# Performance work log

Hardware: AMD Instinct MI355X
Metric: run time of the kernel (lower is better)

The kernel has to match this reference:

```python
import jax, jax.numpy as jnp
import numpy as np

N = 100000   # nodes
E = 1600000  # edges
F = 128      # input features
H = 128      # hidden channels
G = 64       # graphs in batch
EPS = 1e-5   # BatchNorm eps


def setup_inputs() -> dict:
    key = jax.random.key(0)
    ks = jax.random.split(key, 24)
    s = 0.05
    d = {}
    d["x"] = jax.random.normal(ks[0], (N, F), jnp.float32)
    d["edge_index"] = jax.random.randint(ks[1], (2, E), 0, N, dtype=jnp.int32)
    d["batch"] = jnp.sort(jax.random.randint(ks[2], (N,), 0, G, dtype=jnp.int32))
    # GCNConv weights/biases
    d["W1"] = jax.random.normal(ks[3], (F, H), jnp.float32) * s
    d["b1"] = jnp.zeros((H,), jnp.float32)
    d["W2"] = jax.random.normal(ks[4], (H, H), jnp.float32) * s
    d["b2"] = jnp.zeros((H,), jnp.float32)
    d["W3"] = jax.random.normal(ks[5], (H, H), jnp.float32) * s
    d["b3"] = jnp.zeros((H,), jnp.float32)
    # BatchNorm affine params
    for i, k in zip((1, 2, 3), (ks[6], ks[7], ks[8])):
        d[f"g{i}"] = jnp.ones((H,), jnp.float32) + jax.random.normal(k, (H,), jnp.float32) * 0.01
        d[f"be{i}"] = jnp.zeros((H,), jnp.float32)
    # MLP: Linear(2H, H) -> ReLU -> Linear(H, 1)
    d["Wm1"] = jax.random.normal(ks[9], (2 * H, H), jnp.float32) * s
    d["bm1"] = jnp.zeros((H,), jnp.float32)
    d["Wm2"] = jax.random.normal(ks[10], (H, 1), jnp.float32) * s
    d["bm2"] = jnp.zeros((1,), jnp.float32)
    return d


def _gcn_conv(x, W, b, src, dst, dinv):
    # PyG GCNConv: h = D^{-1/2}(A+I)D^{-1/2} (x W) + b, with self-loops
    h = x @ W                                   # [N, H]
    norm = (dinv[src] * dinv[dst])[:, None]     # [E, 1]
    agg = jax.ops.segment_sum(h[src] * norm, dst, num_segments=N)
    agg = agg + h * (dinv * dinv)[:, None]      # self-loop term
    return agg + b


def _bn(x, g, be):
    # BatchNorm1d, training-mode batch stats (biased variance), over node dim
    m = jnp.mean(x, axis=0)
    v = jnp.var(x, axis=0)
    return (x - m) * jax.lax.rsqrt(v + EPS) * g + be


def reference(x, W1, b1, g1, be1, W2, b2, g2, be2, W3, b3, g3, be3,
              Wm1, bm1, Wm2, bm2, edge_index, batch):
    src, dst = edge_index[0], edge_index[1]
    # degree with self-loops (edge weight 1)
    deg = jax.ops.segment_sum(jnp.ones((E,), x.dtype), dst, num_segments=N) + 1.0
    dinv = jax.lax.rsqrt(deg)

    h = jax.nn.relu(_bn(_gcn_conv(x, W1, b1, src, dst, dinv), g1, be1))  # dropout(p=0.05) = identity in eval
    res = h
    h = jax.nn.relu(_bn(_gcn_conv(h, W2, b2, src, dst, dinv), g2, be2)) + res
    res = h
    h = jax.nn.relu(_bn(_gcn_conv(h, W3, b3, src, dst, dinv), g3, be3)) + res

    x_sum = jax.ops.segment_sum(h, batch, num_segments=G)                 # [G, H]
    cnt = jax.ops.segment_sum(jnp.ones((N,), h.dtype), batch, num_segments=G)
    x_mean = x_sum / jnp.maximum(cnt, 1.0)[:, None]
    z = jnp.concatenate([x_sum, x_mean], axis=-1)                         # [G, 2H]
    z = jax.nn.relu(z @ Wm1 + bm1)
    return z @ Wm2 + bm2                                                  # [G, 1]
```

## Files before the change

### kernel.cpp

```cpp
#include <hip/hip_runtime.h>

#define NN 100000
#define EE 1600000
#define HD 128
#define GG 64
#define NB 391
#define BNEPS 1e-5f

typedef unsigned int uint_t;
typedef unsigned short ushort_t;
typedef __attribute__((ext_vector_type(8))) short bf16x8;
typedef __attribute__((ext_vector_type(4))) float f32x4;

static __device__ __forceinline__ ushort_t f2bf(float f){
  uint_t b = __float_as_uint(f);
  return (ushort_t)((b + 0x7FFFu + ((b >> 16) & 1u)) >> 16);
}
static __device__ __forceinline__ uint_t pack2bf(float a, float b){
  return (uint_t)f2bf(a) | ((uint_t)f2bf(b) << 16);
}
static __device__ __forceinline__ float bflo(uint_t u){ return __uint_as_float(u << 16); }
static __device__ __forceinline__ float bfhi(uint_t u){ return __uint_as_float(u & 0xFFFF0000u); }

__global__ void k_hist(const int* __restrict__ ei, int* __restrict__ cnt){
  int e = blockIdx.x*256 + threadIdx.x;
  if (e < EE) atomicAdd(&cnt[ei[EE + e]], 1);
}

__global__ void k_scanA(const int* __restrict__ cnt, int* __restrict__ offs,
                        int* __restrict__ bsum, float* __restrict__ dinv){
  __shared__ int s[256];
  int tid = threadIdx.x;
  int n = blockIdx.x*256 + tid;
  int v = (n < NN) ? cnt[n] : 0;
  if (n < NN) dinv[n] = rsqrtf(1.0f + (float)v);
  s[tid] = v; __syncthreads();
  for (int d = 1; d < 256; d <<= 1){
    int t = (tid >= d) ? s[tid-d] : 0;
    __syncthreads();
    s[tid] += t;
    __syncthreads();
  }
  if (n < NN) offs[n] = s[tid] - v;
  if (tid == 255) bsum[blockIdx.x] = s[255];
}

__global__ void k_scanB(int* __restrict__ bsum){
  __shared__ int s[512];
  int tid = threadIdx.x;
  int v = (tid < NB) ? bsum[tid] : 0;
  s[tid] = v; __syncthreads();
  for (int d = 1; d < 512; d <<= 1){
    int t = (tid >= d) ? s[tid-d] : 0;
    __syncthreads();
    s[tid] += t;
    __syncthreads();
  }
  if (tid < NB) bsum[tid] = s[tid] - v;
}

__global__ void k_scanC(int* __restrict__ offs, const int* __restrict__ bsum){
  int n = blockIdx.x*256 + threadIdx.x;
  if (n < NN) offs[n] += bsum[blockIdx.x];
  if (n == 0) offs[NN] = EE;
}

__global__ void k_scatter(const int* __restrict__ ei, const int* __restrict__ offs,
                          int* __restrict__ cursor, const float* __restrict__ dinv,
                          int2* __restrict__ csr){
  int e = blockIdx.x*256 + threadIdx.x;
  if (e >= EE) return;
  int s = ei[e], d = ei[EE + e];
  int pos = offs[d] + atomicAdd(&cursor[d], 1);
  csr[pos] = make_int2(s, __float_as_int(dinv[s]));
}

__global__ void k_wconv(const float* __restrict__ W, ushort_t* __restrict__ Wt){
  const int c = blockIdx.x, k = threadIdx.x;
  Wt[c*HD + k] = f2bf(W[k*HD + c]);
}

__global__ void __launch_bounds__(256)
k_agg(const ushort_t* __restrict__ hb, const int2* __restrict__ csr,
      const int* __restrict__ offs, const float* __restrict__ dinv,
      const float* __restrict__ bias, float* __restrict__ agg,
      float* __restrict__ bns){
  const int wib  = threadIdx.x >> 6;
  const int lane = threadIdx.x & 63;
  const int gw = blockIdx.x*4 + wib;
  const int nw = gridDim.x*4;
  const int c0 = lane*2;
  const float2 b2 = *(const float2*)&bias[c0];
  float sx=0.f, sy=0.f, qx=0.f, qy=0.f;
  for (int n = gw; n < NN; n += nw){
    const float dn = dinv[n];
    const uint_t hv = *(const uint_t*)&hb[(size_t)n*HD + c0];
    float ax = bflo(hv)*dn, ay = bfhi(hv)*dn;
    const int b0 = offs[n], b1 = offs[n+1];
    int e = b0;
    for (; e + 8 <= b1; e += 8){
      const int2 p0 = csr[e+0];
      const int2 p1 = csr[e+1];
      const int2 p2 = csr[e+2];
      const int2 p3 = csr[e+3];
      const int2 p4 = csr[e+4];
      const int2 p5 = csr[e+5];
      const int2 p6 = csr[e+6];
      const int2 p7 = csr[e+7];
      const uint_t u0 = *(const uint_t*)&hb[(size_t)p0.x*HD + c0];
      const uint_t u1 = *(const uint_t*)&hb[(size_t)p1.x*HD + c0];
      const uint_t u2 = *(const uint_t*)&hb[(size_t)p2.x*HD + c0];
      const uint_t u3 = *(const uint_t*)&hb[(size_t)p3.x*HD + c0];
      const uint_t u4 = *(const uint_t*)&hb[(size_t)p4.x*HD + c0];
      const uint_t u5 = *(const uint_t*)&hb[(size_t)p5.x*HD + c0];
      const uint_t u6 = *(const uint_t*)&hb[(size_t)p6.x*HD + c0];
      const uint_t u7 = *(const uint_t*)&hb[(size_t)p7.x*HD + c0];
      const float w0 = __int_as_float(p0.y), w1 = __int_as_float(p1.y);
      const float w2 = __int_as_float(p2.y), w3 = __int_as_float(p3.y);
      const float w4 = __int_as_float(p4.y), w5 = __int_as_float(p5.y);
      const float w6 = __int_as_float(p6.y), w7 = __int_as_float(p7.y);
      ax = fmaf(bflo(u0), w0, ax); ay = fmaf(bfhi(u0), w0, ay);
      ax = fmaf(bflo(u1), w1, ax); ay = fmaf(bfhi(u1), w1, ay);
      ax = fmaf(bflo(u2), w2, ax); ay = fmaf(bfhi(u2), w2, ay);
      ax = fmaf(bflo(u3), w3, ax); ay = fmaf(bfhi(u3), w3, ay);
      ax = fmaf(bflo(u4), w4, ax); ay = fmaf(bfhi(u4), w4, ay);
      ax = fmaf(bflo(u5), w5, ax); ay = fmaf(bfhi(u5), w5, ay);
      ax = fmaf(bflo(u6), w6, ax); ay = fmaf(bfhi(u6), w6, ay);
      ax = fmaf(bflo(u7), w7, ax); ay = fmaf(bfhi(u7), w7, ay);
    }
    for (; e + 4 <= b1; e += 4){
      const int2 p0 = csr[e+0];
      const int2 p1 = csr[e+1];
      const int2 p2 = csr[e+2];
      const int2 p3 = csr[e+3];
      const uint_t u0 = *(const uint_t*)&hb[(size_t)p0.x*HD + c0];
      const uint_t u1 = *(const uint_t*)&hb[(size_t)p1.x*HD + c0];
      const uint_t u2 = *(const uint_t*)&hb[(size_t)p2.x*HD + c0];
      const uint_t u3 = *(const uint_t*)&hb[(size_t)p3.x*HD + c0];
      const float w0 = __int_as_float(p0.y), w1 = __int_as_float(p1.y);
      const float w2 = __int_as_float(p2.y), w3 = __int_as_float(p3.y);
      ax = fmaf(bflo(u0), w0, ax); ay = fmaf(bfhi(u0), w0, ay);
      ax = fmaf(bflo(u1), w1, ax); ay = fmaf(bfhi(u1), w1, ay);
      ax = fmaf(bflo(u2), w2, ax); ay = fmaf(bfhi(u2), w2, ay);
      ax = fmaf(bflo(u3), w3, ax); ay = fmaf(bfhi(u3), w3, ay);
    }
    for (; e < b1; ++e){
      const int2 p = csr[e];
      const float w = __int_as_float(p.y);
      const uint_t u = *(const uint_t*)&hb[(size_t)p.x*HD + c0];
      ax = fmaf(bflo(u), w, ax);
      ay = fmaf(bfhi(u), w, ay);
    }
    const float ox = fmaf(ax, dn, b2.x);
    const float oy = fmaf(ay, dn, b2.y);
    *(float2*)&agg[(size_t)n*HD + c0] = make_float2(ox, oy);
    sx += ox; sy += oy; qx += ox*ox; qy += oy*oy;
  }
  __shared__ float red[4][64][4];
  red[wib][lane][0]=sx; red[wib][lane][1]=sy; red[wib][lane][2]=qx; red[wib][lane][3]=qy;
  __syncthreads();
  if (wib == 0){
    float a0=0.f,a1=0.f,a2=0.f,a3=0.f;
    #pragma unroll
    for (int w=0; w<4; ++w){
      a0+=red[w][lane][0]; a1+=red[w][lane][1]; a2+=red[w][lane][2]; a3+=red[w][lane][3];
    }
    atomicAdd(&bns[c0  ],    a0);
    atomicAdd(&bns[c0+1],    a1);
    atomicAdd(&bns[HD+c0  ], a2);
    atomicAdd(&bns[HD+c0+1], a3);
  }
}

__global__ void k_bnfin(const float* __restrict__ bns, const float* __restrict__ g,
                        const float* __restrict__ be, float* __restrict__ scale,
                        float* __restrict__ shift){
  int c = threadIdx.x;
  float m = bns[c] * (1.0f/NN);
  float v = bns[HD+c] * (1.0f/NN) - m*m;
  float sc = g[c] * rsqrtf(v + BNEPS);
  scale[c] = sc;
  shift[c] = be[c] - m*sc;
}

template<int MODE>
__global__ void __launch_bounds__(256)
k_rowgemm(const float* __restrict__ A, const float* __restrict__ res,
          const ushort_t* __restrict__ Wt, const float* __restrict__ scale,
          const float* __restrict__ shift,
          ushort_t* __restrict__ HB, float* __restrict__ HOUT){
  __shared__ ushort_t Al[64][136];
  const int tid  = threadIdx.x;
  const int wv   = tid >> 6;
  const int lane = tid & 63;
  const int n0   = blockIdx.x * 64;

  {
    const int r = tid >> 2;
    const int q = tid & 3;
    const int n = n0 + r;
    const int cb = q*32;
    uint_t pk[16];
    if (n < NN){
      #pragma unroll
      for (int j=0;j<8;j++){
        float4 v = *(const float4*)&A[(size_t)n*HD + cb + j*4];
        if (MODE >= 1){
          const float4 sc = *(const float4*)&scale[cb + j*4];
          const float4 sh = *(const float4*)&shift[cb + j*4];
          v.x = fmaxf(fmaf(v.x, sc.x, sh.x), 0.f);
          v.y = fmaxf(fmaf(v.y, sc.y, sh.y), 0.f);
          v.z = fmaxf(fmaf(v.z, sc.z, sh.z), 0.f);
          v.w = fmaxf(fmaf(v.w, sc.w, sh.w), 0.f);
          if (MODE == 2){
            const float4 rv = *(const float4*)&res[(size_t)n*HD + cb + j*4];
            v.x += rv.x; v.y += rv.y; v.z += rv.z; v.w += rv.w;
          }
          *(float4*)&HOUT[(size_t)n*HD + cb + j*4] = v;
        }
        pk[2*j]   = pack2bf(v.x, v.y);
        pk[2*j+1] = pack2bf(v.z, v.w);
      }
    } else {
      #pragma unroll
      for (int i=0;i<16;i++) pk[i] = 0;
    }
    #pragma unroll
    for (int i=0;i<4;i++)
      *(uint4*)&Al[r][cb + i*8] = *(const uint4*)&pk[i*4];
  }
  __syncthreads();

  const int mrow = wv*16 + (lane & 15);
  const int kg8  = (lane >> 4) * 8;
  const int bcol = lane & 15;
  f32x4 acc[8];
  #pragma unroll
  for (int t=0;t<8;t++) acc[t] = (f32x4){0.f,0.f,0.f,0.f};
  #pragma unroll
  for (int ks=0; ks<4; ks++){
    const bf16x8 af = *(const bf16x8*)&Al[mrow][ks*32 + kg8];
    #pragma unroll
    for (int ct=0; ct<8; ct++){
      const bf16x8 bf = *(const bf16x8*)&Wt[(size_t)(ct*16 + bcol)*HD + ks*32 + kg8];
      acc[ct] = __builtin_amdgcn_mfma_f32_16x16x32_bf16(af, bf, acc[ct], 0, 0, 0);
    }
  }

  const int drow = wv*16 + ((lane >> 4) << 2);
  #pragma unroll
  for (int ct=0; ct<8; ct++){
    #pragma unroll
    for (int r=0; r<4; r++){
      const int n = n0 + drow + r;
      if (n < NN) HB[(size_t)n*HD + ct*16 + bcol] = f2bf(acc[ct][r]);
    }
  }
}

__global__ void __launch_bounds__(128)
k_pool(const float* __restrict__ agg, const float* __restrict__ scale,
       const float* __restrict__ shift, const float* __restrict__ h2,
       const int* __restrict__ batch, float* __restrict__ pool,
       float* __restrict__ pcnt){
  const int t = threadIdx.x;
  const int n0 = blockIdx.x*128;
  const float sc = scale[t], sh = shift[t];
  float racc = 0.f;
  int cur = -1, runlen = 0;
  for (int i=0;i<128;i++){
    int n = n0 + i;
    if (n >= NN) break;
    int g = batch[n];
    float v = fmaxf(fmaf(agg[(size_t)n*HD + t], sc, sh), 0.f) + h2[(size_t)n*HD + t];
    if (g != cur){
      if (cur >= 0){
        atomicAdd(&pool[cur*HD + t], racc);
        if (t == 0) atomicAdd(&pcnt[cur], (float)runlen);
      }
      cur = g; racc = 0.f; runlen = 0;
    }
    racc += v; runlen++;
  }
  if (cur >= 0){
    atomicAdd(&pool[cur*HD + t], racc);
    if (t == 0) atomicAdd(&pcnt[cur], (float)runlen);
  }
}

__global__ void __launch_bounds__(128)
k_mlp(const float* __restrict__ pool, const float* __restrict__ pcnt,
      const float* __restrict__ Wm1, const float* __restrict__ bm1,
      const float* __restrict__ Wm2, const float* __restrict__ bm2,
      float* __restrict__ out){
  __shared__ float z[2*HD];
  __shared__ float red[HD];
  const int g = blockIdx.x, t = threadIdx.x;
  float s = pool[g*HD + t];
  float c = fmaxf(pcnt[g], 1.0f);
  z[t] = s; z[HD + t] = s / c;
  __syncthreads();
  float acc = bm1[t];
  for (int i=0;i<2*HD;i++) acc = fmaf(z[i], Wm1[i*HD + t], acc);
  acc = fmaxf(acc, 0.f);
  red[t] = acc * Wm2[t];
  __syncthreads();
  for (int off=64; off>0; off>>=1){
    if (t < off) red[t] += red[t+off];
    __syncthreads();
  }
  if (t == 0) out[g] = red[0] + bm2[0];
}

extern "C" void kernel_launch(void* const* d_in, const int* in_sizes, int n_in,
                              void* d_out, int out_size, void* d_ws, size_t ws_size,
                              hipStream_t stream){
  const float* x   = (const float*)d_in[0];
  const int*  ei   = (const int*)d_in[1];
  const int*  batch= (const int*)d_in[2];
  const float* W1  = (const float*)d_in[3];
  const float* b1  = (const float*)d_in[4];
  const float* W2  = (const float*)d_in[5];
  const float* b2  = (const float*)d_in[6];
  const float* W3  = (const float*)d_in[7];
  const float* b3  = (const float*)d_in[8];
  const float* g1  = (const float*)d_in[9];
  const float* be1 = (const float*)d_in[10];
  const float* g2  = (const float*)d_in[11];
  const float* be2 = (const float*)d_in[12];
  const float* g3  = (const float*)d_in[13];
  const float* be3 = (const float*)d_in[14];
  const float* Wm1 = (const float*)d_in[15];
  const float* bm1 = (const float*)d_in[16];
  const float* Wm2 = (const float*)d_in[17];
  const float* bm2 = (const float*)d_in[18];
  float* out = (float*)d_out;
  (void)in_sizes; (void)n_in; (void)out_size; (void)ws_size;

  char* p = (char*)d_ws;
  auto alloc = [&](size_t bytes)->void*{
    void* r = (void*)p;
    p += (bytes + 511) & ~(size_t)511;
    return r;
  };
  int*   deg    = (int*)  alloc(NN*sizeof(int));
  int*   cursor = (int*)  alloc(NN*sizeof(int));
  float* bns    = (float*)alloc(3*2*HD*sizeof(float));
  float* pool   = (float*)alloc(GG*HD*sizeof(float));
  float* pcnt   = (float*)alloc(GG*sizeof(float));
  size_t zbytes = (size_t)(p - (char*)d_ws);
  int*   offs   = (int*)  alloc((NN+1)*sizeof(int));
  int*   bsum   = (int*)  alloc(512*sizeof(int));
  float* dinv   = (float*)alloc(NN*sizeof(float));
  float* scale  = (float*)alloc(3*HD*sizeof(float));
  float* shift  = (float*)alloc(3*HD*sizeof(float));
  ushort_t* wt1 = (ushort_t*)alloc(HD*HD*sizeof(ushort_t));
  ushort_t* wt2 = (ushort_t*)alloc(HD*HD*sizeof(ushort_t));
  ushort_t* wt3 = (ushort_t*)alloc(HD*HD*sizeof(ushort_t));
  int2*  csr    = (int2*) alloc(((size_t)EE+8)*sizeof(int2));
  ushort_t* hb  = (ushort_t*)alloc((size_t)NN*HD*sizeof(ushort_t));
  float* agg    = (float*)alloc((size_t)NN*HD*sizeof(float));
  float* hres   = (float*)alloc((size_t)NN*HD*sizeof(float));

  hipMemsetAsync(d_ws, 0, zbytes, stream);

  k_hist   <<<(EE+255)/256, 256, 0, stream>>>(ei, deg);
  k_scanA  <<<NB, 256, 0, stream>>>(deg, offs, bsum, dinv);
  k_scanB  <<<1, 512, 0, stream>>>(bsum);
  k_scanC  <<<NB, 256, 0, stream>>>(offs, bsum);
  k_scatter<<<(EE+255)/256, 256, 0, stream>>>(ei, offs, cursor, dinv, csr);
  k_wconv  <<<HD, HD, 0, stream>>>(W1, wt1);
  k_wconv  <<<HD, HD, 0, stream>>>(W2, wt2);
  k_wconv  <<<HD, HD, 0, stream>>>(W3, wt3);

  const int GB = (NN+63)/64;
  k_rowgemm<0><<<GB, 256, 0, stream>>>(x,   nullptr, wt1, nullptr,    nullptr,    hb, nullptr);
  k_agg       <<<2048, 256, 0, stream>>>(hb, csr, offs, dinv, b1, agg, bns);
  k_bnfin     <<<1, 128, 0, stream>>>(bns,        g1, be1, scale,      shift);
  k_rowgemm<1><<<GB, 256, 0, stream>>>(agg, nullptr, wt2, scale,      shift,      hb, hres);
  k_agg       <<<2048, 256, 0, stream>>>(hb, csr, offs, dinv, b2, agg, bns + 2*HD);
  k_bnfin     <<<1, 128, 0, stream>>>(bns + 2*HD, g2, be2, scale+HD,   shift+HD);
  k_rowgemm<2><<<GB, 256, 0, stream>>>(agg, hres,    wt3, scale+HD,   shift+HD,   hb, hres);
  k_agg       <<<2048, 256, 0, stream>>>(hb, csr, offs, dinv, b3, agg, bns + 4*HD);
  k_bnfin     <<<1, 128, 0, stream>>>(bns + 4*HD, g3, be3, scale+2*HD, shift+2*HD);

  k_pool<<<(NN+127)/128, 128, 0, stream>>>(agg, scale+2*HD, shift+2*HD, hres, batch, pool, pcnt);
  k_mlp <<<GG, 128, 0, stream>>>(pool, pcnt, Wm1, bm1, Wm2, bm2, out);
}
```

Baseline: 976.3 us.

## Bin CSR edges by source tile and pre-scale features by dinv in GEMM

Edges are now bucketed per destination node by source-node tile (8 tiles of 12500). The aggregation kernel gives each wave a contiguous block of 13 nodes and sweeps the tiles in order, so gathered rows come from a smaller working set and may reuse L2. The GEMM now pre-multiplies outputs by dinv, so the CSR holds only int indices and the inner loop needs plain adds instead of per-edge weights. The residual buffer is stored in bf16 to cut traffic. In exchange the preprocessing uses more atomics and workspace (8x counters and offsets), the static node partition may balance load worse than the old grid-stride loop, and the bf16 residual adds rounding error.

```diff
diff --git a/kernel.cpp b/kernel.cpp
--- a/kernel.cpp
+++ b/kernel.cpp
@@ -5,6 +5,9 @@
 #define HD 128
 #define GG 64
 #define NB 391
+#define NT 8
+#define TSZ 12500
+#define NPW 13
 #define BNEPS 1e-5f
 
 typedef unsigned int uint_t;
@@ -21,19 +24,27 @@
 }
 static __device__ __forceinline__ float bflo(uint_t u){ return __uint_as_float(u << 16); }
 static __device__ __forceinline__ float bfhi(uint_t u){ return __uint_as_float(u & 0xFFFF0000u); }
-
-__global__ void k_hist(const int* __restrict__ ei, int* __restrict__ cnt){
+static __device__ __forceinline__ float bf1(ushort_t u){ return __uint_as_float(((uint_t)u) << 16); }
+
+__global__ void k_hist2(const int* __restrict__ ei, int* __restrict__ cnt2){
   int e = blockIdx.x*256 + threadIdx.x;
-  if (e < EE) atomicAdd(&cnt[ei[EE + e]], 1);
-}
-
-__global__ void k_scanA(const int* __restrict__ cnt, int* __restrict__ offs,
+  if (e >= EE) return;
+  int s = ei[e], d = ei[EE + e];
+  atomicAdd(&cnt2[d*NT + (uint_t)s/TSZ], 1);
+}
+
+__global__ void k_scanA(const int* __restrict__ cnt2, int* __restrict__ offs,
                         int* __restrict__ bsum, float* __restrict__ dinv){
   __shared__ int s[256];
   int tid = threadIdx.x;
   int n = blockIdx.x*256 + tid;
-  int v = (n < NN) ? cnt[n] : 0;
-  if (n < NN) dinv[n] = rsqrtf(1.0f + (float)v);
+  int v = 0;
+  if (n < NN){
+    const int4 a = *(const int4*)&cnt2[n*NT];
+    const int4 b = *(const int4*)&cnt2[n*NT + 4];
+    v = a.x+a.y+a.z+a.w + b.x+b.y+b.z+b.w;
+    dinv[n] = rsqrtf(1.0f + (float)v);
+  }
   s[tid] = v; __syncthreads();
   for (int d = 1; d < 256; d <<= 1){
     int t = (tid >= d) ? s[tid-d] : 0;
@@ -65,14 +76,27 @@
   if (n == 0) offs[NN] = EE;
 }
 
-__global__ void k_scatter(const int* __restrict__ ei, const int* __restrict__ offs,
-                          int* __restrict__ cursor, const float* __restrict__ dinv,
-                          int2* __restrict__ csr){
+__global__ void k_off2(const int* __restrict__ cnt2, const int* __restrict__ offs,
+                       int* __restrict__ offs2){
+  int n = blockIdx.x*256 + threadIdx.x;
+  if (n >= NN) return;
+  int base = offs[n];
+  #pragma unroll
+  for (int t = 0; t < NT; ++t){
+    offs2[n*NT + t] = base;
+    base += cnt2[n*NT + t];
+  }
+  if (n == 0) offs2[NN*NT] = EE;
+}
+
+__global__ void k_scatter(const int* __restrict__ ei, const int* __restrict__ offs2,
+                          int* __restrict__ cursor2, int* __restrict__ csri){
   int e = blockIdx.x*256 + threadIdx.x;
   if (e >= EE) return;
   int s = ei[e], d = ei[EE + e];
-  int pos = offs[d] + atomicAdd(&cursor[d], 1);
-  csr[pos] = make_int2(s, __float_as_int(dinv[s]));
+  int slot = d*NT + (uint_t)s/TSZ;
+  int pos = offs2[slot] + atomicAdd(&cursor2[slot], 1);
+  csri[pos] = s;
 }
 
 __global__ void k_wconv(const float* __restrict__ W, ushort_t* __restrict__ Wt){
@@ -81,80 +105,63 @@
 }
 
 __global__ void __launch_bounds__(256)
-k_agg(const ushort_t* __restrict__ hb, const int2* __restrict__ csr,
-      const int* __restrict__ offs, const float* __restrict__ dinv,
+k_agg(const ushort_t* __restrict__ hs, const int* __restrict__ csri,
+      const int* __restrict__ offs2, const float* __restrict__ dinv,
       const float* __restrict__ bias, float* __restrict__ agg,
       float* __restrict__ bns){
   const int wib  = threadIdx.x >> 6;
   const int lane = threadIdx.x & 63;
-  const int gw = blockIdx.x*4 + wib;
-  const int nw = gridDim.x*4;
-  const int c0 = lane*2;
+  const int gw   = blockIdx.x*4 + wib;
+  const int c0   = lane*2;
+  const int n0w  = gw*NPW;
+  const int jmax = (n0w < NN) ? min(NPW, NN - n0w) : 0;
+  float2 acc[NPW];
+  #pragma unroll
+  for (int j=0;j<NPW;j++) acc[j] = make_float2(0.f,0.f);
+
+  #pragma unroll 1
+  for (int t = 0; t < NT; ++t){
+    #pragma unroll
+    for (int j = 0; j < NPW; ++j){
+      if (j >= jmax) break;
+      const int n = n0w + j;
+      int e        = offs2[n*NT + t];
+      const int e1 = offs2[n*NT + t + 1];
+      float ax = acc[j].x, ay = acc[j].y;
+      for (; e + 4 <= e1; e += 4){
+        const int s0 = csri[e+0];
+        const int s1 = csri[e+1];
+        const int s2 = csri[e+2];
+        const int s3 = csri[e+3];
+        const uint_t u0 = *(const uint_t*)&hs[(size_t)s0*HD + c0];
+        const uint_t u1 = *(const uint_t*)&hs[(size_t)s1*HD + c0];
+        const uint_t u2 = *(const uint_t*)&hs[(size_t)s2*HD + c0];
+        const uint_t u3 = *(const uint_t*)&hs[(size_t)s3*HD + c0];
+        ax += bflo(u0); ay += bfhi(u0);
+        ax += bflo(u1); ay += bfhi(u1);
+        ax += bflo(u2); ay += bfhi(u2);
+        ax += bflo(u3); ay += bfhi(u3);
+      }
+      for (; e < e1; ++e){
+        const uint_t u = *(const uint_t*)&hs[(size_t)csri[e]*HD + c0];
+        ax += bflo(u); ay += bfhi(u);
+      }
+      acc[j].x = ax; acc[j].y = ay;
+    }
+  }
+
   const float2 b2 = *(const float2*)&bias[c0];
   float sx=0.f, sy=0.f, qx=0.f, qy=0.f;
-  for (int n = gw; n < NN; n += nw){
+  #pragma unroll
+  for (int j = 0; j < NPW; ++j){
+    if (j >= jmax) break;
+    const int n = n0w + j;
     const float dn = dinv[n];
-    const uint_t hv = *(const uint_t*)&hb[(size_t)n*HD + c0];
-    float ax = bflo(hv)*dn, ay = bfhi(hv)*dn;
-    const int b0 = offs[n], b1 = offs[n+1];
-    int e = b0;
-    for (; e + 8 <= b1; e += 8){
-      const int2 p0 = csr[e+0];
-      const int2 p1 = csr[e+1];
-      const int2 p2 = csr[e+2];
-      const int2 p3 = csr[e+3];
-      const int2 p4 = csr[e+4];
-      const int2 p5 = csr[e+5];
-      const int2 p6 = csr[e+6];
-      const int2 p7 = csr[e+7];
-      const uint_t u0 = *(const uint_t*)&hb[(size_t)p0.x*HD + c0];
-      const uint_t u1 = *(const uint_t*)&hb[(size_t)p1.x*HD + c0];
-      const uint_t u2 = *(const uint_t*)&hb[(size_t)p2.x*HD + c0];
-      const uint_t u3 = *(const uint_t*)&hb[(size_t)p3.x*HD + c0];
-      const uint_t u4 = *(const uint_t*)&hb[(size_t)p4.x*HD + c0];
-      const uint_t u5 = *(const uint_t*)&hb[(size_t)p5.x*HD + c0];
-      const uint_t u6 = *(const uint_t*)&hb[(size_t)p6.x*HD + c0];
-      const uint_t u7 = *(const uint_t*)&hb[(size_t)p7.x*HD + c0];
-      const float w0 = __int_as_float(p0.y), w1 = __int_as_float(p1.y);
-      const float w2 = __int_as_float(p2.y), w3 = __int_as_float(p3.y);
-      const float w4 = __int_as_float(p4.y), w5 = __int_as_float(p5.y);
-      const float w6 = __int_as_float(p6.y), w7 = __int_as_float(p7.y);
-      ax = fmaf(bflo(u0), w0, ax); ay = fmaf(bfhi(u0), w0, ay);
-      ax = fmaf(bflo(u1), w1, ax); ay = fmaf(bfhi(u1), w1, ay);
-      ax = fmaf(bflo(u2), w2, ax); ay = fmaf(bfhi(u2), w2, ay);
-      ax = fmaf(bflo(u3), w3, ax); ay = fmaf(bfhi(u3), w3, ay);
-      ax = fmaf(bflo(u4), w4, ax); ay = fmaf(bfhi(u4), w4, ay);
-      ax = fmaf(bflo(u5), w5, ax); ay = fmaf(bfhi(u5), w5, ay);
-      ax = fmaf(bflo(u6), w6, ax); ay = fmaf(bfhi(u6), w6, ay);
-      ax = fmaf(bflo(u7), w7, ax); ay = fmaf(bfhi(u7), w7, ay);
-    }
-    for (; e + 4 <= b1; e += 4){
-      const int2 p0 = csr[e+0];
-      const int2 p1 = csr[e+1];
-      const int2 p2 = csr[e+2];
-      const int2 p3 = csr[e+3];
-      const uint_t u0 = *(const uint_t*)&hb[(size_t)p0.x*HD + c0];
-      const uint_t u1 = *(const uint_t*)&hb[(size_t)p1.x*HD + c0];
-      const uint_t u2 = *(const uint_t*)&hb[(size_t)p2.x*HD + c0];
-      const uint_t u3 = *(const uint_t*)&hb[(size_t)p3.x*HD + c0];
-      const float w0 = __int_as_float(p0.y), w1 = __int_as_float(p1.y);
-      const float w2 = __int_as_float(p2.y), w3 = __int_as_float(p3.y);
-      ax = fmaf(bflo(u0), w0, ax); ay = fmaf(bfhi(u0), w0, ay);
-      ax = fmaf(bflo(u1), w1, ax); ay = fmaf(bfhi(u1), w1, ay);
-      ax = fmaf(bflo(u2), w2, ax); ay = fmaf(bfhi(u2), w2, ay);
-      ax = fmaf(bflo(u3), w3, ax); ay = fmaf(bfhi(u3), w3, ay);
-    }
-    for (; e < b1; ++e){
-      const int2 p = csr[e];
-      const float w = __int_as_float(p.y);
-      const uint_t u = *(const uint_t*)&hb[(size_t)p.x*HD + c0];
-      ax = fmaf(bflo(u), w, ax);
-      ay = fmaf(bfhi(u), w, ay);
-    }
-    const float ox = fmaf(ax, dn, b2.x);
-    const float oy = fmaf(ay, dn, b2.y);
+    const uint_t hv = *(const uint_t*)&hs[(size_t)n*HD + c0];
+    const float ox = fmaf(acc[j].x + bflo(hv), dn, b2.x);
+    const float oy = fmaf(acc[j].y + bfhi(hv), dn, b2.y);
     *(float2*)&agg[(size_t)n*HD + c0] = make_float2(ox, oy);
-    sx += ox; sy += oy; qx += ox*ox; qy += oy*oy;
+    sx += ox; sy += oy; qx = fmaf(ox,ox,qx); qy = fmaf(oy,oy,qy);
   }
   __shared__ float red[4][64][4];
   red[wib][lane][0]=sx; red[wib][lane][1]=sy; red[wib][lane][2]=qx; red[wib][lane][3]=qy;
@@ -185,10 +192,10 @@
 
 template<int MODE>
 __global__ void __launch_bounds__(256)
-k_rowgemm(const float* __restrict__ A, const float* __restrict__ res,
+k_rowgemm(const float* __restrict__ A, const ushort_t* __restrict__ res,
           const ushort_t* __restrict__ Wt, const float* __restrict__ scale,
-          const float* __restrict__ shift,
-          ushort_t* __restrict__ HB, float* __restrict__ HOUT){
+          const float* __restrict__ shift, const float* __restrict__ dinv,
+          ushort_t* __restrict__ HS, ushort_t* __restrict__ HOUT){
   __shared__ ushort_t Al[64][136];
   const int tid  = threadIdx.x;
   const int wv   = tid >> 6;
@@ -213,10 +220,12 @@
           v.z = fmaxf(fmaf(v.z, sc.z, sh.z), 0.f);
           v.w = fmaxf(fmaf(v.w, sc.w, sh.w), 0.f);
           if (MODE == 2){
-            const float4 rv = *(const float4*)&res[(size_t)n*HD + cb + j*4];
-            v.x += rv.x; v.y += rv.y; v.z += rv.z; v.w += rv.w;
+            const uint2 rv = *(const uint2*)&res[(size_t)n*HD + cb + j*4];
+            v.x += bflo(rv.x); v.y += bfhi(rv.x);
+            v.z += bflo(rv.y); v.w += bfhi(rv.y);
           }
-          *(float4*)&HOUT[(size_t)n*HD + cb + j*4] = v;
+          *(uint2*)&HOUT[(size_t)n*HD + cb + j*4] =
+            make_uint2(pack2bf(v.x, v.y), pack2bf(v.z, v.w));
         }
         pk[2*j]   = pack2bf(v.x, v.y);
         pk[2*j+1] = pack2bf(v.z, v.w);
@@ -248,19 +257,25 @@
   }
 
   const int drow = wv*16 + ((lane >> 4) << 2);
+  float dv[4];
+  #pragma unroll
+  for (int r=0;r<4;r++){
+    const int n = n0 + drow + r;
+    dv[r] = (n < NN) ? dinv[n] : 0.f;
+  }
   #pragma unroll
   for (int ct=0; ct<8; ct++){
     #pragma unroll
     for (int r=0; r<4; r++){
       const int n = n0 + drow + r;
-      if (n < NN) HB[(size_t)n*HD + ct*16 + bcol] = f2bf(acc[ct][r]);
+      if (n < NN) HS[(size_t)n*HD + ct*16 + bcol] = f2bf(acc[ct][r] * dv[r]);
     }
   }
 }
 
 __global__ void __launch_bounds__(128)
 k_pool(const float* __restrict__ agg, const float* __restrict__ scale,
-       const float* __restrict__ shift, const float* __restrict__ h2,
+       const float* __restrict__ shift, const ushort_t* __restrict__ h2,
        const int* __restrict__ batch, float* __restrict__ pool,
        float* __restrict__ pcnt){
   const int t = threadIdx.x;
@@ -272,7 +287,7 @@
     int n = n0 + i;
     if (n >= NN) break;
     int g = batch[n];
-    float v = fmaxf(fmaf(agg[(size_t)n*HD + t], sc, sh), 0.f) + h2[(size_t)n*HD + t];
+    float v = fmaxf(fmaf(agg[(size_t)n*HD + t], sc, sh), 0.f) + bf1(h2[(size_t)n*HD + t]);
     if (g != cur){
       if (cur >= 0){
         atomicAdd(&pool[cur*HD + t], racc);
@@ -343,13 +358,14 @@
     p += (bytes + 511) & ~(size_t)511;
     return r;
   };
-  int*   deg    = (int*)  alloc(NN*sizeof(int));
-  int*   cursor = (int*)  alloc(NN*sizeof(int));
-  float* bns    = (float*)alloc(3*2*HD*sizeof(float));
-  float* pool   = (float*)alloc(GG*HD*sizeof(float));
-  float* pcnt   = (float*)alloc(GG*sizeof(float));
+  int*   cnt2    = (int*)  alloc((size_t)NN*NT*sizeof(int));
+  int*   cursor2 = (int*)  alloc((size_t)NN*NT*sizeof(int));
+  float* bns     = (float*)alloc(3*2*HD*sizeof(float));
+  float* pool    = (float*)alloc(GG*HD*sizeof(float));
+  float* pcnt    = (float*)alloc(GG*sizeof(float));
   size_t zbytes = (size_t)(p - (char*)d_ws);
   int*   offs   = (int*)  alloc((NN+1)*sizeof(int));
+  int*   offs2  = (int*)  alloc(((size_t)NN*NT+1)*sizeof(int));
   int*   bsum   = (int*)  alloc(512*sizeof(int));
   float* dinv   = (float*)alloc(NN*sizeof(float));
   float* scale  = (float*)alloc(3*HD*sizeof(float));
@@ -357,31 +373,32 @@
   ushort_t* wt1 = (ushort_t*)alloc(HD*HD*sizeof(ushort_t));
   ushort_t* wt2 = (ushort_t*)alloc(HD*HD*sizeof(ushort_t));
   ushort_t* wt3 = (ushort_t*)alloc(HD*HD*sizeof(ushort_t));
-  int2*  csr    = (int2*) alloc(((size_t)EE+8)*sizeof(int2));
-  ushort_t* hb  = (ushort_t*)alloc((size_t)NN*HD*sizeof(ushort_t));
+  int*   csri   = (int*)  alloc(((size_t)EE+8)*sizeof(int));
+  ushort_t* hs  = (ushort_t*)alloc((size_t)NN*HD*sizeof(ushort_t));
   float* agg    = (float*)alloc((size_t)NN*HD*sizeof(float));
-  float* hres   = (float*)alloc((size_t)NN*HD*sizeof(float));
+  ushort_t* hres= (ushort_t*)alloc((size_t)NN*HD*sizeof(ushort_t));
 
   hipMemsetAsync(d_ws, 0, zbytes, stream);
 
-  k_hist   <<<(EE+255)/256, 256, 0, stream>>>(ei, deg);
-  k_scanA  <<<NB, 256, 0, stream>>>(deg, offs, bsum, dinv);
+  k_hist2  <<<(EE+255)/256, 256, 0, stream>>>(ei, cnt2);
+  k_scanA  <<<NB, 256, 0, stream>>>(cnt2, offs, bsum, dinv);
   k_scanB  <<<1, 512, 0, stream>>>(bsum);
   k_scanC  <<<NB, 256, 0, stream>>>(offs, bsum);
-  k_scatter<<<(EE+255)/256, 256, 0, stream>>>(ei, offs, cursor, dinv, csr);
+  k_off2   <<<NB, 256, 0, stream>>>(cnt2, offs, offs2);
+  k_scatter<<<(EE+255)/256, 256, 0, stream>>>(ei, offs2, cursor2, csri);
   k_wconv  <<<HD, HD, 0, stream>>>(W1, wt1);
   k_wconv  <<<HD, HD, 0, stream>>>(W2, wt2);
   k_wconv  <<<HD, HD, 0, stream>>>(W3, wt3);
 
   const int GB = (NN+63)/64;
-  k_rowgemm<0><<<GB, 256, 0, stream>>>(x,   nullptr, wt1, nullptr,    nullptr,    hb, nullptr);
-  k_agg       <<<2048, 256, 0, stream>>>(hb, csr, offs, dinv, b1, agg, bns);
+  k_rowgemm<0><<<GB, 256, 0, stream>>>(x,   nullptr, wt1, nullptr,    nullptr,    dinv, hs, nullptr);
+  k_agg       <<<2048, 256, 0, stream>>>(hs, csri, offs2, dinv, b1, agg, bns);
   k_bnfin     <<<1, 128, 0, stream>>>(bns,        g1, be1, scale,      shift);
-  k_rowgemm<1><<<GB, 256, 0, stream>>>(agg, nullptr, wt2, scale,      shift,      hb, hres);
-  k_agg       <<<2048, 256, 0, stream>>>(hb, csr, offs, dinv, b2, agg, bns + 2*HD);
+  k_rowgemm<1><<<GB, 256, 0, stream>>>(agg, nullptr, wt2, scale,      shift,      dinv, hs, hres);
+  k_agg       <<<2048, 256, 0, stream>>>(hs, csri, offs2, dinv, b2, agg, bns + 2*HD);
   k_bnfin     <<<1, 128, 0, stream>>>(bns + 2*HD, g2, be2, scale+HD,   shift+HD);
-  k_rowgemm<2><<<GB, 256, 0, stream>>>(agg, hres,    wt3, scale+HD,   shift+HD,   hb, hres);
-  k_agg       <<<2048, 256, 0, stream>>>(hb, csr, offs, dinv, b3, agg, bns + 4*HD);
+  k_rowgemm<2><<<GB, 256, 0, stream>>>(agg, hres,    wt3, scale+HD,   shift+HD,   dinv, hs, hres);
+  k_agg       <<<2048, 256, 0, stream>>>(hs, csri, offs2, dinv, b3, agg, bns + 4*HD);
   k_bnfin     <<<1, 128, 0, stream>>>(bns + 4*HD, g3, be3, scale+2*HD, shift+2*HD);
 
   k_pool<<<(NN+127)/128, 128, 0, stream>>>(agg, scale+2*HD, shift+2*HD, hres, batch, pool, pcnt);
```

New measurement: 1.337 ms. 1.37x slower.
